# Optimization experiments

Hardware: AMD Instinct MI355X
Metric: run time of the kernel (lower is better)

## Reference

```python
import jax, jax.numpy as jnp
import numpy as np

N_NODES = 100000
N_EDGES = 3200000
IN_DIM = 256
HID_DIM = 64
OUT_DIM = 64


def setup_inputs() -> dict:
    key = jax.random.key(0)
    k1, k2, k3, k4, k5, k6 = jax.random.split(key, 6)
    x = jax.random.normal(k1, (N_NODES, IN_DIM), dtype=jnp.float32)
    edge_index = jax.random.randint(k2, (2, N_EDGES), 0, N_NODES, dtype=jnp.int32)
    # Glorot-style init for the two GCNConv layers (PyG default: glorot weight, zero bias)
    W1 = jax.random.normal(k3, (IN_DIM, HID_DIM), dtype=jnp.float32) * (1.0 / np.sqrt(IN_DIM))
    b1 = jnp.zeros((HID_DIM,), dtype=jnp.float32)
    W2 = jax.random.normal(k4, (HID_DIM, OUT_DIM), dtype=jnp.float32) * (1.0 / np.sqrt(HID_DIM))
    b2 = jnp.zeros((OUT_DIM,), dtype=jnp.float32)
    return {"x": x, "edge_index": edge_index, "W1": W1, "b1": b1, "W2": W2, "b2": b2}


def _gcn_conv(x, src, dst, deg_inv_sqrt, W, b, n):
    # PyG GCNConv: h = x W; out_i = sum_j norm_ij * h_j + b, with symmetric norm
    h = x @ W                                   # (n, d_out) small GEMM
    norm = deg_inv_sqrt[src] * deg_inv_sqrt[dst]  # (E+n,)
    msg = norm[:, None] * h[src]                # gather (E+n, d_out)
    agg = jax.ops.segment_sum(msg, dst, num_segments=n)  # scatter-add
    return agg + b


def reference(x, edge_index, W1, b1, W2, b2):
    n = x.shape[0]
    loops = jnp.arange(n, dtype=edge_index.dtype)
    src = jnp.concatenate([edge_index[0], loops])
    dst = jnp.concatenate([edge_index[1], loops])
    # degree on destination (col) with added self-loops, weight 1.0
    deg = jax.ops.segment_sum(jnp.ones_like(dst, dtype=x.dtype), dst, num_segments=n)
    deg_inv_sqrt = jnp.where(deg > 0, jax.lax.rsqrt(deg), 0.0)
    h = jax.nn.relu(_gcn_conv(x, src, dst, deg_inv_sqrt, W1, b1, n))
    return _gcn_conv(h, src, dst, deg_inv_sqrt, W2, b2, n)
```

## Files before the change

### kernel.cpp

```cpp
#include <hip/hip_runtime.h>
#include <cstdint>
#include <cstddef>


#define BIN_SHIFT 7
#define BIN_NODES 128
#define MAX_BINS 1024
#define SUP_SHIFT 11
#define FINE_PER_SUP 16
#define NSUP_MAX 64
#define SCAP 56
#define SRC_BITS 17
#define SRC_MASK ((1 << SRC_BITS) - 1)

typedef unsigned short ushort_t;

typedef __attribute__((ext_vector_type(8))) short bf16x8;
typedef __attribute__((ext_vector_type(4))) float f32x4;

union FragB {
  uint4 u;
  bf16x8 b;
};

__device__ __forceinline__ float4 bfq2f4(uint2 p) {
  float4 r;
  r.x = __uint_as_float(p.x << 16);
  r.y = __uint_as_float(p.x & 0xFFFF0000u);
  r.z = __uint_as_float(p.y << 16);
  r.w = __uint_as_float(p.y & 0xFFFF0000u);
  return r;
}
__device__ __forceinline__ unsigned f2bf(float f) {
  unsigned u = __float_as_uint(f);
  return (u + 0x7FFFu + ((u >> 16) & 1u)) >> 16;
}
__device__ __forceinline__ uint2 f42bfq(float4 f) {
  uint2 r;
  r.x = f2bf(f.x) | (f2bf(f.y) << 16);
  r.y = f2bf(f.z) | (f2bf(f.w) << 16);
  return r;
}

__global__ void zero_int(int* __restrict__ p, int n) {
  int i = blockIdx.x * blockDim.x + threadIdx.x;
  if (i < n) p[i] = 0;
}

__global__ __launch_bounds__(256) void bin_count(const int* __restrict__ dst, int E, int nbins,
                                                 int* __restrict__ binCnt) {
  __shared__ int h[MAX_BINS];
  for (int i = threadIdx.x; i < nbins; i += 256) h[i] = 0;
  __syncthreads();
  int stride = gridDim.x * 256;
  for (int e = blockIdx.x * 256 + threadIdx.x; e < E; e += stride)
    atomicAdd(&h[dst[e] >> BIN_SHIFT], 1);
  __syncthreads();
  for (int i = threadIdx.x; i < nbins; i += 256)
    if (h[i]) atomicAdd(&binCnt[i], h[i]);
}

__global__ __launch_bounds__(256) void bin_scan(const int* __restrict__ binCnt, int nbins, int E,
                                                int* __restrict__ binStart,
                                                int* __restrict__ binCursor,
                                                int* __restrict__ supCursor) {
  __shared__ int s[256];
  int t = threadIdx.x;
  int c[4];
  int sum = 0;
#pragma unroll
  for (int i = 0; i < 4; i++) {
    int idx = t * 4 + i;
    c[i] = (idx < nbins) ? binCnt[idx] : 0;
    sum += c[i];
  }
  int v = sum;
  s[t] = v;
  __syncthreads();
  for (int d = 1; d < 256; d <<= 1) {
    int add = (t >= d) ? s[t - d] : 0;
    __syncthreads();
    s[t] += add;
    __syncthreads();
  }
  int run = s[t] - v;
#pragma unroll
  for (int i = 0; i < 4; i++) {
    int idx = t * 4 + i;
    if (idx < nbins) {
      binStart[idx] = run;
      binCursor[idx] = run;
      if ((idx & (FINE_PER_SUP - 1)) == 0) supCursor[idx >> 4] = run;
      run += c[i];
    }
  }
  if (t == 0) binStart[nbins] = E;
}

__global__ __launch_bounds__(256) void super_fill(const int* __restrict__ src,
                                                  const int* __restrict__ dst, int E, int nsup,
                                                  int* __restrict__ supCursor,
                                                  unsigned* __restrict__ supbuf) {
  __shared__ unsigned stage[NSUP_MAX * SCAP];
  __shared__ int lcnt[NSUP_MAX], lbase[NSUP_MAX], lscan[NSUP_MAX + 1];
  const int tid = threadIdx.x;
  const int t0 = blockIdx.x * 2048;
  const int t1 = min(E, t0 + 2048);

  int dv[8], sv[8];
#pragma unroll
  for (int i = 0; i < 8; i++) {
    int e = t0 + i * 256 + tid;
    if (e < t1) {
      dv[i] = dst[e];
      sv[i] = src[e];
    }
  }
  if (tid < nsup) lcnt[tid] = 0;
  __syncthreads();
#pragma unroll
  for (int i = 0; i < 8; i++) {
    int e = t0 + i * 256 + tid;
    if (e < t1) {
      int d = dv[i];
      int sb = d >> SUP_SHIFT;
      unsigned v = ((unsigned)(d & ((1 << SUP_SHIFT) - 1)) << SRC_BITS) | (unsigned)sv[i];
      int idx = atomicAdd(&lcnt[sb], 1);
      if (idx < SCAP)
        stage[sb * SCAP + idx] = v;
      else {
        int g = atomicAdd(&supCursor[sb], 1);
        supbuf[g] = v;
      }
    }
  }
  __syncthreads();
  if (tid < nsup) {
    int c = min(lcnt[tid], SCAP);
    lcnt[tid] = c;
    lbase[tid] = c ? atomicAdd(&supCursor[tid], c) : 0;
  }
  __syncthreads();
  if (tid < 64) {
    int vv = (tid < nsup) ? lcnt[tid] : 0;
    int ss = vv;
#pragma unroll
    for (int d = 1; d < 64; d <<= 1) {
      int u = __shfl_up(ss, d);
      if (tid >= d) ss += u;
    }
    lscan[tid + 1] = ss;
    if (tid == 0) lscan[0] = 0;
  }
  __syncthreads();
  int total = lscan[nsup];
  for (int j = tid; j < total; j += 256) {
    int lo = 0, hi = nsup;
    while (hi - lo > 1) {
      int mid = (lo + hi) >> 1;
      if (lscan[mid] <= j)
        lo = mid;
      else
        hi = mid;
    }
    int off = j - lscan[lo];
    supbuf[lbase[lo] + off] = stage[lo * SCAP + off];
  }
}

__global__ __launch_bounds__(256) void fine_fill(const unsigned* __restrict__ supbuf,
                                                 const int* __restrict__ binStart, int nbins,
                                                 int* __restrict__ binCursor,
                                                 unsigned* __restrict__ binbuf) {
  __shared__ int lcnt[FINE_PER_SUP], lbase[FINE_PER_SUP];
  int sb = blockIdx.x >> 3, p = blockIdx.x & 7;
  int seg0 = binStart[sb << 4];
  int seg1 = binStart[min((sb + 1) << 4, nbins)];
  int part = (seg1 - seg0 + 7) >> 3;
  int c0 = seg0 + p * part;
  int c1 = min(seg1, c0 + part);
  if (threadIdx.x < FINE_PER_SUP) lcnt[threadIdx.x] = 0;
  __syncthreads();
  for (int i = c0 + threadIdx.x; i < c1; i += 256) atomicAdd(&lcnt[supbuf[i] >> 24], 1);
  __syncthreads();
  if (threadIdx.x < FINE_PER_SUP) {
    int c = lcnt[threadIdx.x];
    lbase[threadIdx.x] = c ? atomicAdd(&binCursor[(sb << 4) + threadIdx.x], c) : 0;
    lcnt[threadIdx.x] = 0;
  }
  __syncthreads();
  for (int i = c0 + threadIdx.x; i < c1; i += 256) {
    unsigned v = supbuf[i];
    unsigned dls = v >> SRC_BITS;
    int f = dls >> BIN_SHIFT;
    unsigned vf = ((dls & (BIN_NODES - 1)) << SRC_BITS) | (v & SRC_MASK);
    int idx = lbase[f] + atomicAdd(&lcnt[f], 1);
    binbuf[idx] = vf;
  }
}

__global__ __launch_bounds__(256) void node_count_dis(const unsigned* __restrict__ binbuf,
                                                      const int* __restrict__ binStart, int N,
                                                      int* __restrict__ count,
                                                      float* __restrict__ dis) {
  __shared__ int cnt[BIN_NODES];
  int b = blockIdx.x;
  int nodeBase = b << BIN_SHIFT;
  if (threadIdx.x < BIN_NODES) cnt[threadIdx.x] = 0;
  __syncthreads();
  int s0 = binStart[b], s1 = binStart[b + 1];
  for (int i = s0 + threadIdx.x; i < s1; i += 256) atomicAdd(&cnt[binbuf[i] >> SRC_BITS], 1);
  __syncthreads();
  if (threadIdx.x < BIN_NODES) {
    int node = nodeBase + threadIdx.x;
    if (node < N) {
      int c = cnt[threadIdx.x];
      count[node] = c;
      dis[node] = rsqrtf((float)(c + 1));
    }
  }
}

__global__ __launch_bounds__(256) void bin_csr(const unsigned* __restrict__ binbuf,
                                               const int* __restrict__ binStart,
                                               const int* __restrict__ count, int N, int E,
                                               int* __restrict__ rowptr, int* __restrict__ col) {
  __shared__ int cur[BIN_NODES];
  __shared__ int pref[BIN_NODES];
  int b = blockIdx.x, t = threadIdx.x;
  int nodeBase = b << BIN_SHIFT;
  int c = 0;
  if (t < BIN_NODES) {
    int node = nodeBase + t;
    c = (node < N) ? count[node] : 0;
    pref[t] = c;
  }
  __syncthreads();
  for (int d = 1; d < BIN_NODES; d <<= 1) {
    int add = (t < BIN_NODES && t >= d) ? pref[t - d] : 0;
    __syncthreads();
    if (t < BIN_NODES) pref[t] += add;
    __syncthreads();
  }
  int s0 = binStart[b];
  if (t < BIN_NODES) {
    int node = nodeBase + t;
    if (node < N) {
      int ex = s0 + pref[t] - c;
      rowptr[node] = ex;
      cur[t] = ex;
    }
  }
  if (b == 0 && t == 255) rowptr[N] = E;
  __syncthreads();
  int s1 = binStart[b + 1];
  for (int i = s0 + t; i < s1; i += 256) {
    unsigned v = binbuf[i];
    int slot = atomicAdd(&cur[v >> SRC_BITS], 1);
    col[slot] = v & SRC_MASK;
  }
}

__global__ __launch_bounds__(256) void wsplit(const float* __restrict__ W1,
                                              const float* __restrict__ W2,
                                              ushort_t* __restrict__ wt1,
                                              ushort_t* __restrict__ wt2) {
  int i = blockIdx.x * 256 + threadIdx.x;
  const float* W;
  ushort_t* wt;
  int K, idx;
  if (i < 256 * 64) {
    W = W1; wt = wt1; K = 256; idx = i;
  } else if (i < 256 * 64 + 64 * 64) {
    W = W2; wt = wt2; K = 64; idx = i - 256 * 64;
  } else
    return;
  int n = idx & 63, k = idx >> 6;
  float f = W[k * 64 + n];
  unsigned u = __float_as_uint(f);
  unsigned hb = u & 0xFFFF0000u;
  float lo = f - __uint_as_float(hb);
  wt[(size_t)n * K + k] = (ushort_t)(u >> 16);
  wt[(size_t)64 * K + (size_t)n * K + k] = (ushort_t)(__float_as_uint(lo) >> 16);
}

__device__ __forceinline__ void split8u(uint4 a, uint4 b, uint4& xh, uint4& xl) {
  unsigned ua[8] = {a.x, a.y, a.z, a.w, b.x, b.y, b.z, b.w};
  unsigned hw[4], lw[4];
#pragma unroll
  for (int p = 0; p < 4; p++) {
    unsigned u0 = ua[2 * p], u1 = ua[2 * p + 1];
    unsigned h0 = u0 & 0xFFFF0000u, h1 = u1 & 0xFFFF0000u;
    float l0 = __uint_as_float(u0) - __uint_as_float(h0);
    float l1 = __uint_as_float(u1) - __uint_as_float(h1);
    hw[p] = (u0 >> 16) | h1;
    lw[p] = (__float_as_uint(l0) >> 16) | (__float_as_uint(l1) & 0xFFFF0000u);
  }
  xh = make_uint4(hw[0], hw[1], hw[2], hw[3]);
  xl = make_uint4(lw[0], lw[1], lw[2], lw[3]);
}

__global__ __launch_bounds__(256, 3) void gemm1_mfma(const float* __restrict__ A,
                                                     const ushort_t* __restrict__ Wt,
                                                     uint2* __restrict__ Cb, int M) {
  constexpr int K = 256;
  __shared__ uint4 xtile[3][4][256];
  const int lane = threadIdx.x & 63;
  const int wv = threadIdx.x >> 6;
  const int l15 = lane & 15;
  const int lq = lane >> 4;
  const int m0 = blockIdx.x * 128 + wv * 32;

  const ushort_t* __restrict__ Wlo = Wt + (size_t)64 * K;

  f32x4 acc[2][4];
#pragma unroll
  for (int a = 0; a < 2; a++)
#pragma unroll
    for (int b = 0; b < 4; b++) acc[a][b] = (f32x4){0.f, 0.f, 0.f, 0.f};

  auto stage_tile = [&](int kt, int buf) {
#pragma unroll
    for (int c = 0; c < 4; c++) {
      int s = c * 64 + lane;
      int r = s >> 3;
      int c4 = (s & 7) ^ (r & 7);
      int nd = m0 + r;
      if (nd >= M) nd = M - 1;
      const float* gp = A + (size_t)nd * K + kt * 32 + c4 * 4;
      __builtin_amdgcn_global_load_lds(
          (const __attribute__((address_space(1))) void*)gp,
          (__attribute__((address_space(3))) void*)&xtile[buf][wv][c * 64], 16, 0, 0);
    }
  };

  stage_tile(0, 0);
  stage_tile(1, 1);
  __builtin_amdgcn_sched_barrier(0);

#pragma unroll
  for (int j = 0; j < 8; j++) {
    FragB w[8];
    {
      const int kb = j * 32 + lq * 8;
#pragma unroll
      for (int nt = 0; nt < 4; nt++) {
        w[nt].u = *(const uint4*)(Wt + (size_t)(nt * 16 + l15) * K + kb);
        w[4 + nt].u = *(const uint4*)(Wlo + (size_t)(nt * 16 + l15) * K + kb);
      }
    }
    __builtin_amdgcn_sched_barrier(0);
    if (j < 7)
      asm volatile("s_waitcnt vmcnt(12)" ::: "memory");
    else
      asm volatile("s_waitcnt vmcnt(8)" ::: "memory");
    __builtin_amdgcn_sched_barrier(0);
    uint4 xa[2][2];
#pragma unroll
    for (int mt = 0; mt < 2; mt++) {
      int mr = mt * 16 + l15;
#pragma unroll
      for (int hh = 0; hh < 2; hh++) {
        int c4 = (lq * 2 + hh) ^ (mr & 7);
        xa[mt][hh] = *(const uint4*)&xtile[j % 3][wv][mr * 8 + c4];
      }
    }
    __builtin_amdgcn_sched_barrier(0);
    if (j + 2 < 8) stage_tile(j + 2, (j + 2) % 3);
    __builtin_amdgcn_sched_barrier(0);
    FragB xh0, xl0, xh1, xl1;
    split8u(xa[0][0], xa[0][1], xh0.u, xl0.u);
    split8u(xa[1][0], xa[1][1], xh1.u, xl1.u);
#pragma unroll
    for (int nt = 0; nt < 4; nt++) {
      acc[0][nt] = __builtin_amdgcn_mfma_f32_16x16x32_bf16(w[nt].b, xh0.b, acc[0][nt], 0, 0, 0);
      acc[0][nt] = __builtin_amdgcn_mfma_f32_16x16x32_bf16(w[nt].b, xl0.b, acc[0][nt], 0, 0, 0);
      acc[1][nt] = __builtin_amdgcn_mfma_f32_16x16x32_bf16(w[nt].b, xh1.b, acc[1][nt], 0, 0, 0);
      acc[1][nt] = __builtin_amdgcn_mfma_f32_16x16x32_bf16(w[nt].b, xl1.b, acc[1][nt], 0, 0, 0);
    }
#pragma unroll
    for (int nt = 0; nt < 4; nt++) {
      acc[0][nt] = __builtin_amdgcn_mfma_f32_16x16x32_bf16(w[4 + nt].b, xh0.b, acc[0][nt], 0, 0, 0);
      acc[1][nt] = __builtin_amdgcn_mfma_f32_16x16x32_bf16(w[4 + nt].b, xh1.b, acc[1][nt], 0, 0, 0);
    }
  }

#pragma unroll
  for (int mt = 0; mt < 2; mt++) {
    int node = m0 + mt * 16 + l15;
    if (node < M) {
      uint2* cp = Cb + (size_t)node * 16 + lq;
#pragma unroll
      for (int nt = 0; nt < 4; nt++) {
        float4 o = make_float4(acc[mt][nt][0], acc[mt][nt][1], acc[mt][nt][2], acc[mt][nt][3]);
        cp[nt * 4] = f42bfq(o);
      }
    }
  }
}

__global__ __launch_bounds__(256, 3) void gemm2_mfma(const ushort_t* __restrict__ Av,
                                                     const ushort_t* __restrict__ Wt,
                                                     uint2* __restrict__ Cb, int M) {
  constexpr int K = 64;
  constexpr int NT = K / 32;
  const int lane = threadIdx.x & 63;
  const int wv = threadIdx.x >> 6;
  const int l15 = lane & 15;
  const int lq = lane >> 4;
  const int m0 = blockIdx.x * 128 + wv * 32;

  const ushort_t* __restrict__ Wlo = Wt + (size_t)64 * K;

  f32x4 acc[2][4];
#pragma unroll
  for (int a = 0; a < 2; a++)
#pragma unroll
    for (int b = 0; b < 4; b++) acc[a][b] = (f32x4){0.f, 0.f, 0.f, 0.f};

  int node[2], ncl[2];
#pragma unroll
  for (int mt = 0; mt < 2; mt++) {
    node[mt] = m0 + mt * 16 + l15;
    ncl[mt] = node[mt] < M ? node[mt] : (M - 1);
  }

  FragB xa[NT][2], wh[NT][4], wl[NT][4];
#pragma unroll
  for (int t = 0; t < NT; t++)
#pragma unroll
    for (int mt = 0; mt < 2; mt++)
      xa[t][mt].u = *(const uint4*)(Av + (size_t)ncl[mt] * K + t * 32 + lq * 8);
#pragma unroll
  for (int t = 0; t < NT; t++)
#pragma unroll
    for (int nt = 0; nt < 4; nt++) {
      wh[t][nt].u = *(const uint4*)(Wt + (size_t)(nt * 16 + l15) * K + t * 32 + lq * 8);
      wl[t][nt].u = *(const uint4*)(Wlo + (size_t)(nt * 16 + l15) * K + t * 32 + lq * 8);
    }
#pragma unroll
  for (int t = 0; t < NT; t++)
#pragma unroll
    for (int mt = 0; mt < 2; mt++)
#pragma unroll
      for (int nt = 0; nt < 4; nt++) {
        acc[mt][nt] =
            __builtin_amdgcn_mfma_f32_16x16x32_bf16(wh[t][nt].b, xa[t][mt].b, acc[mt][nt], 0, 0, 0);
        acc[mt][nt] =
            __builtin_amdgcn_mfma_f32_16x16x32_bf16(wl[t][nt].b, xa[t][mt].b, acc[mt][nt], 0, 0, 0);
      }

#pragma unroll
  for (int mt = 0; mt < 2; mt++) {
    if (node[mt] < M) {
      uint2* cp = Cb + (size_t)node[mt] * 16 + lq;
#pragma unroll
      for (int nt = 0; nt < 4; nt++) {
        float4 o = make_float4(acc[mt][nt][0], acc[mt][nt][1], acc[mt][nt][2], acc[mt][nt][3]);
        cp[nt * 4] = f42bfq(o);
      }
    }
  }
}

template <bool OUTBF>
__global__ __launch_bounds__(256) void agg_kernel(
    const uint2* __restrict__ h, const int* __restrict__ rowptr, const int* __restrict__ col,
    const float* __restrict__ dis, const float* __restrict__ bias, void* __restrict__ outv,
    int N, int relu) {
  int wid = (blockIdx.x * blockDim.x + threadIdx.x) >> 6;
  if (wid >= N) return;
  int lane = threadIdx.x & 63;
  int sub = lane & 15;
  int quarter = lane >> 4;

  int start = rowptr[wid], end = rowptr[wid + 1];
  float di = dis[wid];

  float4 a0 = make_float4(0.f, 0.f, 0.f, 0.f), a1 = a0, a2 = a0, a3 = a0;
  {
    float4 self = bfq2f4(h[(size_t)wid * 16 + sub]);
    if (quarter == 0) {
      a0.x = di * self.x;
      a0.y = di * self.y;
      a0.z = di * self.z;
      a0.w = di * self.w;
    }
  }

  for (int base = start; base < end; base += 64) {
    int e = base + lane;
    int sj = 0;
    float wj = 0.f;
    if (e < end) {
      sj = col[e];
      wj = dis[sj];
    }
    int cnt = end - base;
    if (cnt > 64) cnt = 64;
    int rounds = (cnt + 3) >> 2;

    uint2 g0, g1, g2, g3;
    float w0, w1, w2, w3;
#define ISSUE(gi, G, W)                                              \
  do {                                                               \
    int _i = (4 * (gi) + quarter) & 63;                              \
    int _s = __shfl(sj, _i);                                         \
    float _w = __shfl(wj, _i);                                       \
    if ((gi) < rounds) {                                             \
      G = h[(size_t)_s * 16 + sub];                                  \
      W = _w;                                                        \
    } else {                                                         \
      G = make_uint2(0u, 0u);                                        \
      W = 0.f;                                                       \
    }                                                                \
  } while (0)

    ISSUE(0, g0, w0);
    ISSUE(1, g1, w1);
    ISSUE(2, g2, w2);
    ISSUE(3, g3, w3);
    int rounds4 = (rounds + 3) & ~3;
    for (int t0 = 0; t0 < rounds4; t0 += 4) {
      {
        float4 gf = bfq2f4(g0);
        a0.x += w0 * gf.x; a0.y += w0 * gf.y; a0.z += w0 * gf.z; a0.w += w0 * gf.w;
      }
      ISSUE(t0 + 4, g0, w0);
      {
        float4 gf = bfq2f4(g1);
        a1.x += w1 * gf.x; a1.y += w1 * gf.y; a1.z += w1 * gf.z; a1.w += w1 * gf.w;
      }
      ISSUE(t0 + 5, g1, w1);
      {
        float4 gf = bfq2f4(g2);
        a2.x += w2 * gf.x; a2.y += w2 * gf.y; a2.z += w2 * gf.z; a2.w += w2 * gf.w;
      }
      ISSUE(t0 + 6, g2, w2);
      {
        float4 gf = bfq2f4(g3);
        a3.x += w3 * gf.x; a3.y += w3 * gf.y; a3.z += w3 * gf.z; a3.w += w3 * gf.w;
      }
      ISSUE(t0 + 7, g3, w3);
    }
#undef ISSUE
  }

  float sx = (a0.x + a1.x) + (a2.x + a3.x);
  float sy = (a0.y + a1.y) + (a2.y + a3.y);
  float sz = (a0.z + a1.z) + (a2.z + a3.z);
  float sw = (a0.w + a1.w) + (a2.w + a3.w);
  sx += __shfl_down(sx, 32); sy += __shfl_down(sy, 32);
  sz += __shfl_down(sz, 32); sw += __shfl_down(sw, 32);
  sx += __shfl_down(sx, 16); sy += __shfl_down(sy, 16);
  sz += __shfl_down(sz, 16); sw += __shfl_down(sw, 16);
  if (quarter == 0) {
    float4 bv = ((const float4*)bias)[sub];
    float4 o = make_float4(di * sx + bv.x, di * sy + bv.y, di * sz + bv.z, di * sw + bv.w);
    if (relu) {
      o.x = fmaxf(o.x, 0.f);
      o.y = fmaxf(o.y, 0.f);
      o.z = fmaxf(o.z, 0.f);
      o.w = fmaxf(o.w, 0.f);
    }
    if (OUTBF)
      ((uint2*)outv)[(size_t)wid * 16 + sub] = f42bfq(o);
    else
      ((float4*)outv)[(size_t)wid * 16 + sub] = o;
  }
}

extern "C" void kernel_launch(void* const* d_in, const int* in_sizes, int n_in,
                              void* d_out, int out_size, void* d_ws, size_t ws_size,
                              hipStream_t stream) {
  const float* x = (const float*)d_in[0];
  const int* ei = (const int*)d_in[1];
  const float* W1 = (const float*)d_in[2];
  const float* b1 = (const float*)d_in[3];
  const float* W2 = (const float*)d_in[4];
  const float* b2 = (const float*)d_in[5];

  const int IN = 256;
  const int E = in_sizes[1] / 2;
  const int N = in_sizes[0] / IN;
  const int* src = ei;
  const int* dst = ei + E;
  const int nbins = (N + BIN_NODES - 1) >> BIN_SHIFT;
  const int nsup = (N + (1 << SUP_SHIFT) - 1) >> SUP_SHIFT;

  char* ws = (char*)d_ws;
  size_t off = 0;
  auto alloc = [&](size_t bytes) -> void* {
    void* p = ws + off;
    off += (bytes + 255) & ~(size_t)255;
    return p;
  };
  int* count = (int*)alloc((size_t)N * 4);
  int* rowptr = (int*)alloc((size_t)(N + 1) * 4);
  float* dis = (float*)alloc((size_t)N * 4);
  int* binCnt = (int*)alloc(MAX_BINS * 4);
  int* binStart = (int*)alloc((MAX_BINS + 1) * 4);
  int* binCursor = (int*)alloc(MAX_BINS * 4);
  int* supCursor = (int*)alloc(NSUP_MAX * 4);
  int* col = (int*)alloc((size_t)E * 4);
  unsigned* supbuf = (unsigned*)col;
  uint2* out1 = (uint2*)alloc((size_t)N * 64 * 2);
  size_t big = ((size_t)E * 4 > (size_t)N * 128) ? (size_t)E * 4 : (size_t)N * 128;
  unsigned* binbuf = (unsigned*)alloc(big);
  uint2* h = (uint2*)binbuf;
  ushort_t* wt1 = (ushort_t*)alloc((size_t)2 * 64 * 256 * 2);
  ushort_t* wt2 = (ushort_t*)alloc((size_t)2 * 64 * 64 * 2);
  float* outf = (float*)d_out;

  zero_int<<<(nbins + 255) / 256, 256, 0, stream>>>(binCnt, nbins);
  bin_count<<<1024, 256, 0, stream>>>(dst, E, nbins, binCnt);
  bin_scan<<<1, 256, 0, stream>>>(binCnt, nbins, E, binStart, binCursor, supCursor);
  super_fill<<<(E + 2047) / 2048, 256, 0, stream>>>(src, dst, E, nsup, supCursor, supbuf);
  fine_fill<<<nsup * 8, 256, 0, stream>>>(supbuf, binStart, nbins, binCursor, binbuf);
  node_count_dis<<<nbins, 256, 0, stream>>>(binbuf, binStart, N, count, dis);
  bin_csr<<<nbins, 256, 0, stream>>>(binbuf, binStart, count, N, E, rowptr, col);
  wsplit<<<(256 * 64 + 64 * 64 + 255) / 256, 256, 0, stream>>>(W1, W2, wt1, wt2);

  gemm1_mfma<<<(N + 127) / 128, 256, 0, stream>>>(x, wt1, h, N);
  agg_kernel<true><<<(N + 3) / 4, 256, 0, stream>>>(h, rowptr, col, dis, b1, out1, N, 1);
  gemm2_mfma<<<(N + 127) / 128, 256, 0, stream>>>((const ushort_t*)out1, wt2, h, N);
  agg_kernel<false><<<(N + 3) / 4, 256, 0, stream>>>(h, rowptr, col, dis, b2, outf, N, 0);
}
```

Before: 461.3 us.

## Fuse node count into CSR build and shrink GEMM row tiles to 16 per wave

Merges node_count_dis into bin_csr, so per-node counts are computed in shared memory and the count array plus one kernel launch and one pass over binbuf are removed. Both MFMA GEMM kernels now give each wave 16 rows instead of 32 and each block 64 rows, with half-size LDS tiles and launch bounds raised to 4 blocks per CU. The smaller tiles are meant to add occupancy and blocks for latency hiding, at the cost of reloading the weight fragments for twice as many blocks and less reuse of each weight load.

```diff
diff --git a/kernel.cpp b/kernel.cpp
--- a/kernel.cpp
+++ b/kernel.cpp
@@ -199,40 +199,27 @@
   }
 }
 
-__global__ __launch_bounds__(256) void node_count_dis(const unsigned* __restrict__ binbuf,
-                                                      const int* __restrict__ binStart, int N,
-                                                      int* __restrict__ count,
-                                                      float* __restrict__ dis) {
+__global__ __launch_bounds__(256) void bin_csr(const unsigned* __restrict__ binbuf,
+                                               const int* __restrict__ binStart, int N, int E,
+                                               int* __restrict__ rowptr, int* __restrict__ col,
+                                               float* __restrict__ dis) {
   __shared__ int cnt[BIN_NODES];
-  int b = blockIdx.x;
-  int nodeBase = b << BIN_SHIFT;
-  if (threadIdx.x < BIN_NODES) cnt[threadIdx.x] = 0;
-  __syncthreads();
-  int s0 = binStart[b], s1 = binStart[b + 1];
-  for (int i = s0 + threadIdx.x; i < s1; i += 256) atomicAdd(&cnt[binbuf[i] >> SRC_BITS], 1);
-  __syncthreads();
-  if (threadIdx.x < BIN_NODES) {
-    int node = nodeBase + threadIdx.x;
-    if (node < N) {
-      int c = cnt[threadIdx.x];
-      count[node] = c;
-      dis[node] = rsqrtf((float)(c + 1));
-    }
-  }
-}
-
-__global__ __launch_bounds__(256) void bin_csr(const unsigned* __restrict__ binbuf,
-                                               const int* __restrict__ binStart,
-                                               const int* __restrict__ count, int N, int E,
-                                               int* __restrict__ rowptr, int* __restrict__ col) {
   __shared__ int cur[BIN_NODES];
   __shared__ int pref[BIN_NODES];
   int b = blockIdx.x, t = threadIdx.x;
   int nodeBase = b << BIN_SHIFT;
+  if (t < BIN_NODES) cnt[t] = 0;
+  __syncthreads();
+  int s0 = binStart[b], s1 = binStart[b + 1];
+  for (int i = s0 + t; i < s1; i += 256) atomicAdd(&cnt[binbuf[i] >> SRC_BITS], 1);
+  __syncthreads();
   int c = 0;
   if (t < BIN_NODES) {
     int node = nodeBase + t;
-    c = (node < N) ? count[node] : 0;
+    if (node < N) {
+      c = cnt[t];
+      dis[node] = rsqrtf((float)(c + 1));
+    }
     pref[t] = c;
   }
   __syncthreads();
@@ -242,7 +229,6 @@
     if (t < BIN_NODES) pref[t] += add;
     __syncthreads();
   }
-  int s0 = binStart[b];
   if (t < BIN_NODES) {
     int node = nodeBase + t;
     if (node < N) {
@@ -253,7 +239,6 @@
   }
   if (b == 0 && t == 255) rowptr[N] = E;
   __syncthreads();
-  int s1 = binStart[b + 1];
   for (int i = s0 + t; i < s1; i += 256) {
     unsigned v = binbuf[i];
     int slot = atomicAdd(&cur[v >> SRC_BITS], 1);
@@ -300,28 +285,26 @@
   xl = make_uint4(lw[0], lw[1], lw[2], lw[3]);
 }
 
-__global__ __launch_bounds__(256, 3) void gemm1_mfma(const float* __restrict__ A,
+__global__ __launch_bounds__(256, 4) void gemm1_mfma(const float* __restrict__ A,
                                                      const ushort_t* __restrict__ Wt,
                                                      uint2* __restrict__ Cb, int M) {
   constexpr int K = 256;
-  __shared__ uint4 xtile[3][4][256];
+  __shared__ uint4 xtile[3][4][128];
   const int lane = threadIdx.x & 63;
   const int wv = threadIdx.x >> 6;
   const int l15 = lane & 15;
   const int lq = lane >> 4;
-  const int m0 = blockIdx.x * 128 + wv * 32;
+  const int m0 = blockIdx.x * 64 + wv * 16;
 
   const ushort_t* __restrict__ Wlo = Wt + (size_t)64 * K;
 
-  f32x4 acc[2][4];
-#pragma unroll
-  for (int a = 0; a < 2; a++)
-#pragma unroll
-    for (int b = 0; b < 4; b++) acc[a][b] = (f32x4){0.f, 0.f, 0.f, 0.f};
+  f32x4 acc[4];
+#pragma unroll
+  for (int b = 0; b < 4; b++) acc[b] = (f32x4){0.f, 0.f, 0.f, 0.f};
 
   auto stage_tile = [&](int kt, int buf) {
 #pragma unroll
-    for (int c = 0; c < 4; c++) {
+    for (int c = 0; c < 2; c++) {
       int s = c * 64 + lane;
       int r = s >> 3;
       int c4 = (s & 7) ^ (r & 7);
@@ -351,55 +334,46 @@
     }
     __builtin_amdgcn_sched_barrier(0);
     if (j < 7)
-      asm volatile("s_waitcnt vmcnt(12)" ::: "memory");
+      asm volatile("s_waitcnt vmcnt(10)" ::: "memory");
     else
       asm volatile("s_waitcnt vmcnt(8)" ::: "memory");
     __builtin_amdgcn_sched_barrier(0);
-    uint4 xa[2][2];
-#pragma unroll
-    for (int mt = 0; mt < 2; mt++) {
-      int mr = mt * 16 + l15;
-#pragma unroll
-      for (int hh = 0; hh < 2; hh++) {
-        int c4 = (lq * 2 + hh) ^ (mr & 7);
-        xa[mt][hh] = *(const uint4*)&xtile[j % 3][wv][mr * 8 + c4];
-      }
+    uint4 xa[2];
+#pragma unroll
+    for (int hh = 0; hh < 2; hh++) {
+      int c4 = (lq * 2 + hh) ^ (l15 & 7);
+      xa[hh] = *(const uint4*)&xtile[j % 3][wv][l15 * 8 + c4];
     }
     __builtin_amdgcn_sched_barrier(0);
     if (j + 2 < 8) stage_tile(j + 2, (j + 2) % 3);
     __builtin_amdgcn_sched_barrier(0);
-    FragB xh0, xl0, xh1, xl1;
-    split8u(xa[0][0], xa[0][1], xh0.u, xl0.u);
-    split8u(xa[1][0], xa[1][1], xh1.u, xl1.u);
+    FragB xh0, xl0;
+    split8u(xa[0], xa[1], xh0.u, xl0.u);
 #pragma unroll
     for (int nt = 0; nt < 4; nt++) {
-      acc[0][nt] = __builtin_amdgcn_mfma_f32_16x16x32_bf16(w[nt].b, xh0.b, acc[0][nt], 0, 0, 0);
-      acc[0][nt] = __builtin_amdgcn_mfma_f32_16x16x32_bf16(w[nt].b, xl0.b, acc[0][nt], 0, 0, 0);
-      acc[1][nt] = __builtin_amdgcn_mfma_f32_16x16x32_bf16(w[nt].b, xh1.b, acc[1][nt], 0, 0, 0);
-      acc[1][nt] = __builtin_amdgcn_mfma_f32_16x16x32_bf16(w[nt].b, xl1.b, acc[1][nt], 0, 0, 0);
+      acc[nt] = __builtin_amdgcn_mfma_f32_16x16x32_bf16(w[nt].b, xh0.b, acc[nt], 0, 0, 0);
+      acc[nt] = __builtin_amdgcn_mfma_f32_16x16x32_bf16(w[nt].b, xl0.b, acc[nt], 0, 0, 0);
     }
 #pragma unroll
     for (int nt = 0; nt < 4; nt++) {
-      acc[0][nt] = __builtin_amdgcn_mfma_f32_16x16x32_bf16(w[4 + nt].b, xh0.b, acc[0][nt], 0, 0, 0);
-      acc[1][nt] = __builtin_amdgcn_mfma_f32_16x16x32_bf16(w[4 + nt].b, xh1.b, acc[1][nt], 0, 0, 0);
-    }
-  }
-
-#pragma unroll
-  for (int mt = 0; mt < 2; mt++) {
-    int node = m0 + mt * 16 + l15;
+      acc[nt] = __builtin_amdgcn_mfma_f32_16x16x32_bf16(w[4 + nt].b, xh0.b, acc[nt], 0, 0, 0);
+    }
+  }
+
+  {
+    int node = m0 + l15;
     if (node < M) {
       uint2* cp = Cb + (size_t)node * 16 + lq;
 #pragma unroll
       for (int nt = 0; nt < 4; nt++) {
-        float4 o = make_float4(acc[mt][nt][0], acc[mt][nt][1], acc[mt][nt][2], acc[mt][nt][3]);
+        float4 o = make_float4(acc[nt][0], acc[nt][1], acc[nt][2], acc[nt][3]);
         cp[nt * 4] = f42bfq(o);
       }
     }
   }
 }
 
-__global__ __launch_bounds__(256, 3) void gemm2_mfma(const ushort_t* __restrict__ Av,
+__global__ __launch_bounds__(256, 4) void gemm2_mfma(const ushort_t* __restrict__ Av,
                                                      const ushort_t* __restrict__ Wt,
                                                      uint2* __restrict__ Cb, int M) {
   constexpr int K = 64;
@@ -408,29 +382,21 @@
   const int wv = threadIdx.x >> 6;
   const int l15 = lane & 15;
   const int lq = lane >> 4;
-  const int m0 = blockIdx.x * 128 + wv * 32;
+  const int m0 = blockIdx.x * 64 + wv * 16;
 
   const ushort_t* __restrict__ Wlo = Wt + (size_t)64 * K;
 
-  f32x4 acc[2][4];
-#pragma unroll
-  for (int a = 0; a < 2; a++)
-#pragma unroll
-    for (int b = 0; b < 4; b++) acc[a][b] = (f32x4){0.f, 0.f, 0.f, 0.f};
-
-  int node[2], ncl[2];
-#pragma unroll
-  for (int mt = 0; mt < 2; mt++) {
-    node[mt] = m0 + mt * 16 + l15;
-    ncl[mt] = node[mt] < M ? node[mt] : (M - 1);
-  }
-
-  FragB xa[NT][2], wh[NT][4], wl[NT][4];
+  f32x4 acc[4];
+#pragma unroll
+  for (int b = 0; b < 4; b++) acc[b] = (f32x4){0.f, 0.f, 0.f, 0.f};
+
+  int node = m0 + l15;
+  int ncl = node < M ? node : (M - 1);
+
+  FragB xa[NT], wh[NT][4], wl[NT][4];
 #pragma unroll
   for (int t = 0; t < NT; t++)
-#pragma unroll
-    for (int mt = 0; mt < 2; mt++)
-      xa[t][mt].u = *(const uint4*)(Av + (size_t)ncl[mt] * K + t * 32 + lq * 8);
+    xa[t].u = *(const uint4*)(Av + (size_t)ncl * K + t * 32 + lq * 8);
 #pragma unroll
   for (int t = 0; t < NT; t++)
 #pragma unroll
@@ -441,24 +407,17 @@
 #pragma unroll
   for (int t = 0; t < NT; t++)
 #pragma unroll
-    for (int mt = 0; mt < 2; mt++)
-#pragma unroll
-      for (int nt = 0; nt < 4; nt++) {
-        acc[mt][nt] =
-            __builtin_amdgcn_mfma_f32_16x16x32_bf16(wh[t][nt].b, xa[t][mt].b, acc[mt][nt], 0, 0, 0);
-        acc[mt][nt] =
-            __builtin_amdgcn_mfma_f32_16x16x32_bf16(wl[t][nt].b, xa[t][mt].b, acc[mt][nt], 0, 0, 0);
-      }
-
-#pragma unroll
-  for (int mt = 0; mt < 2; mt++) {
-    if (node[mt] < M) {
-      uint2* cp = Cb + (size_t)node[mt] * 16 + lq;
-#pragma unroll
-      for (int nt = 0; nt < 4; nt++) {
-        float4 o = make_float4(acc[mt][nt][0], acc[mt][nt][1], acc[mt][nt][2], acc[mt][nt][3]);
-        cp[nt * 4] = f42bfq(o);
-      }
+    for (int nt = 0; nt < 4; nt++) {
+      acc[nt] = __builtin_amdgcn_mfma_f32_16x16x32_bf16(wh[t][nt].b, xa[t].b, acc[nt], 0, 0, 0);
+      acc[nt] = __builtin_amdgcn_mfma_f32_16x16x32_bf16(wl[t][nt].b, xa[t].b, acc[nt], 0, 0, 0);
+    }
+
+  if (node < M) {
+    uint2* cp = Cb + (size_t)node * 16 + lq;
+#pragma unroll
+    for (int nt = 0; nt < 4; nt++) {
+      float4 o = make_float4(acc[nt][0], acc[nt][1], acc[nt][2], acc[nt][3]);
+      cp[nt * 4] = f42bfq(o);
     }
   }
 }
@@ -595,7 +554,6 @@
     off += (bytes + 255) & ~(size_t)255;
     return p;
   };
-  int* count = (int*)alloc((size_t)N * 4);
   int* rowptr = (int*)alloc((size_t)(N + 1) * 4);
   float* dis = (float*)alloc((size_t)N * 4);
   int* binCnt = (int*)alloc(MAX_BINS * 4);
@@ -617,12 +575,11 @@
   bin_scan<<<1, 256, 0, stream>>>(binCnt, nbins, E, binStart, binCursor, supCursor);
   super_fill<<<(E + 2047) / 2048, 256, 0, stream>>>(src, dst, E, nsup, supCursor, supbuf);
   fine_fill<<<nsup * 8, 256, 0, stream>>>(supbuf, binStart, nbins, binCursor, binbuf);
-  node_count_dis<<<nbins, 256, 0, stream>>>(binbuf, binStart, N, count, dis);
-  bin_csr<<<nbins, 256, 0, stream>>>(binbuf, binStart, count, N, E, rowptr, col);
+  bin_csr<<<nbins, 256, 0, stream>>>(binbuf, binStart, N, E, rowptr, col, dis);
   wsplit<<<(256 * 64 + 64 * 64 + 255) / 256, 256, 0, stream>>>(W1, W2, wt1, wt2);
 
-  gemm1_mfma<<<(N + 127) / 128, 256, 0, stream>>>(x, wt1, h, N);
+  gemm1_mfma<<<(N + 63) / 64, 256, 0, stream>>>(x, wt1, h, N);
   agg_kernel<true><<<(N + 3) / 4, 256, 0, stream>>>(h, rowptr, col, dis, b1, out1, N, 1);
-  gemm2_mfma<<<(N + 127) / 128, 256, 0, stream>>>((const ushort_t*)out1, wt2, h, N);
+  gemm2_mfma<<<(N + 63) / 64, 256, 0, stream>>>((const ushort_t*)out1, wt2, h, N);
   agg_kernel<false><<<(N + 3) / 4, 256, 0, stream>>>(h, rowptr, col, dis, b2, outf, N, 0);
 }
```

Result: slower. 477.2 us (+3.5%).

## Fuse degree count into CSR build and enlarge gemm1 tile to 256 rows

Applied to the files above, without the earlier changes.

Merges the node_count_dis kernel into bin_csr, so per-node counts are computed in shared memory and the count array round trip and one launch go away. gemm1 now processes 64 rows per wave (256 per block), reusing each weight fragment across four M-tiles instead of two. It switches from triple to double buffering with an explicit LDS wait before restaging, and lowers the occupancy hint to two blocks. This costs more registers and less latency hiding per block, in exchange for fewer weight reloads per row.

```diff
diff --git a/kernel.cpp b/kernel.cpp
--- a/kernel.cpp
+++ b/kernel.cpp
@@ -199,40 +199,27 @@
   }
 }
 
-__global__ __launch_bounds__(256) void node_count_dis(const unsigned* __restrict__ binbuf,
-                                                      const int* __restrict__ binStart, int N,
-                                                      int* __restrict__ count,
-                                                      float* __restrict__ dis) {
+__global__ __launch_bounds__(256) void bin_csr(const unsigned* __restrict__ binbuf,
+                                               const int* __restrict__ binStart, int N, int E,
+                                               int* __restrict__ rowptr, int* __restrict__ col,
+                                               float* __restrict__ dis) {
   __shared__ int cnt[BIN_NODES];
-  int b = blockIdx.x;
-  int nodeBase = b << BIN_SHIFT;
-  if (threadIdx.x < BIN_NODES) cnt[threadIdx.x] = 0;
-  __syncthreads();
-  int s0 = binStart[b], s1 = binStart[b + 1];
-  for (int i = s0 + threadIdx.x; i < s1; i += 256) atomicAdd(&cnt[binbuf[i] >> SRC_BITS], 1);
-  __syncthreads();
-  if (threadIdx.x < BIN_NODES) {
-    int node = nodeBase + threadIdx.x;
-    if (node < N) {
-      int c = cnt[threadIdx.x];
-      count[node] = c;
-      dis[node] = rsqrtf((float)(c + 1));
-    }
-  }
-}
-
-__global__ __launch_bounds__(256) void bin_csr(const unsigned* __restrict__ binbuf,
-                                               const int* __restrict__ binStart,
-                                               const int* __restrict__ count, int N, int E,
-                                               int* __restrict__ rowptr, int* __restrict__ col) {
   __shared__ int cur[BIN_NODES];
   __shared__ int pref[BIN_NODES];
   int b = blockIdx.x, t = threadIdx.x;
   int nodeBase = b << BIN_SHIFT;
+  if (t < BIN_NODES) cnt[t] = 0;
+  __syncthreads();
+  int s0 = binStart[b], s1 = binStart[b + 1];
+  for (int i = s0 + t; i < s1; i += 256) atomicAdd(&cnt[binbuf[i] >> SRC_BITS], 1);
+  __syncthreads();
   int c = 0;
   if (t < BIN_NODES) {
     int node = nodeBase + t;
-    c = (node < N) ? count[node] : 0;
+    if (node < N) {
+      c = cnt[t];
+      dis[node] = rsqrtf((float)(c + 1));
+    }
     pref[t] = c;
   }
   __syncthreads();
@@ -242,7 +229,6 @@
     if (t < BIN_NODES) pref[t] += add;
     __syncthreads();
   }
-  int s0 = binStart[b];
   if (t < BIN_NODES) {
     int node = nodeBase + t;
     if (node < N) {
@@ -253,7 +239,6 @@
   }
   if (b == 0 && t == 255) rowptr[N] = E;
   __syncthreads();
-  int s1 = binStart[b + 1];
   for (int i = s0 + t; i < s1; i += 256) {
     unsigned v = binbuf[i];
     int slot = atomicAdd(&cur[v >> SRC_BITS], 1);
@@ -300,28 +285,28 @@
   xl = make_uint4(lw[0], lw[1], lw[2], lw[3]);
 }
 
-__global__ __launch_bounds__(256, 3) void gemm1_mfma(const float* __restrict__ A,
+__global__ __launch_bounds__(256, 2) void gemm1_mfma(const float* __restrict__ A,
                                                      const ushort_t* __restrict__ Wt,
                                                      uint2* __restrict__ Cb, int M) {
   constexpr int K = 256;
-  __shared__ uint4 xtile[3][4][256];
+  __shared__ uint4 xtile[2][4][512];
   const int lane = threadIdx.x & 63;
   const int wv = threadIdx.x >> 6;
   const int l15 = lane & 15;
   const int lq = lane >> 4;
-  const int m0 = blockIdx.x * 128 + wv * 32;
+  const int m0 = blockIdx.x * 256 + wv * 64;
 
   const ushort_t* __restrict__ Wlo = Wt + (size_t)64 * K;
 
-  f32x4 acc[2][4];
-#pragma unroll
-  for (int a = 0; a < 2; a++)
+  f32x4 acc[4][4];
+#pragma unroll
+  for (int a = 0; a < 4; a++)
 #pragma unroll
     for (int b = 0; b < 4; b++) acc[a][b] = (f32x4){0.f, 0.f, 0.f, 0.f};
 
   auto stage_tile = [&](int kt, int buf) {
 #pragma unroll
-    for (int c = 0; c < 4; c++) {
+    for (int c = 0; c < 8; c++) {
       int s = c * 64 + lane;
       int r = s >> 3;
       int c4 = (s & 7) ^ (r & 7);
@@ -351,42 +336,44 @@
     }
     __builtin_amdgcn_sched_barrier(0);
     if (j < 7)
-      asm volatile("s_waitcnt vmcnt(12)" ::: "memory");
+      asm volatile("s_waitcnt vmcnt(16)" ::: "memory");
     else
       asm volatile("s_waitcnt vmcnt(8)" ::: "memory");
     __builtin_amdgcn_sched_barrier(0);
-    uint4 xa[2][2];
-#pragma unroll
-    for (int mt = 0; mt < 2; mt++) {
+    uint4 xa[4][2];
+#pragma unroll
+    for (int mt = 0; mt < 4; mt++) {
       int mr = mt * 16 + l15;
 #pragma unroll
       for (int hh = 0; hh < 2; hh++) {
         int c4 = (lq * 2 + hh) ^ (mr & 7);
-        xa[mt][hh] = *(const uint4*)&xtile[j % 3][wv][mr * 8 + c4];
+        xa[mt][hh] = *(const uint4*)&xtile[j & 1][wv][mr * 8 + c4];
       }
     }
     __builtin_amdgcn_sched_barrier(0);
-    if (j + 2 < 8) stage_tile(j + 2, (j + 2) % 3);
+    asm volatile("s_waitcnt lgkmcnt(0)" ::: "memory");
     __builtin_amdgcn_sched_barrier(0);
-    FragB xh0, xl0, xh1, xl1;
-    split8u(xa[0][0], xa[0][1], xh0.u, xl0.u);
-    split8u(xa[1][0], xa[1][1], xh1.u, xl1.u);
-#pragma unroll
-    for (int nt = 0; nt < 4; nt++) {
-      acc[0][nt] = __builtin_amdgcn_mfma_f32_16x16x32_bf16(w[nt].b, xh0.b, acc[0][nt], 0, 0, 0);
-      acc[0][nt] = __builtin_amdgcn_mfma_f32_16x16x32_bf16(w[nt].b, xl0.b, acc[0][nt], 0, 0, 0);
-      acc[1][nt] = __builtin_amdgcn_mfma_f32_16x16x32_bf16(w[nt].b, xh1.b, acc[1][nt], 0, 0, 0);
-      acc[1][nt] = __builtin_amdgcn_mfma_f32_16x16x32_bf16(w[nt].b, xl1.b, acc[1][nt], 0, 0, 0);
-    }
-#pragma unroll
-    for (int nt = 0; nt < 4; nt++) {
-      acc[0][nt] = __builtin_amdgcn_mfma_f32_16x16x32_bf16(w[4 + nt].b, xh0.b, acc[0][nt], 0, 0, 0);
-      acc[1][nt] = __builtin_amdgcn_mfma_f32_16x16x32_bf16(w[4 + nt].b, xh1.b, acc[1][nt], 0, 0, 0);
-    }
-  }
-
-#pragma unroll
-  for (int mt = 0; mt < 2; mt++) {
+    if (j + 2 < 8) stage_tile(j + 2, j & 1);
+    __builtin_amdgcn_sched_barrier(0);
+#pragma unroll
+    for (int mt = 0; mt < 4; mt++) {
+      FragB xh, xl;
+      split8u(xa[mt][0], xa[mt][1], xh.u, xl.u);
+#pragma unroll
+      for (int nt = 0; nt < 4; nt++) {
+        acc[mt][nt] = __builtin_amdgcn_mfma_f32_16x16x32_bf16(w[nt].b, xh.b, acc[mt][nt], 0, 0, 0);
+        acc[mt][nt] = __builtin_amdgcn_mfma_f32_16x16x32_bf16(w[nt].b, xl.b, acc[mt][nt], 0, 0, 0);
+      }
+#pragma unroll
+      for (int nt = 0; nt < 4; nt++) {
+        acc[mt][nt] =
+            __builtin_amdgcn_mfma_f32_16x16x32_bf16(w[4 + nt].b, xh.b, acc[mt][nt], 0, 0, 0);
+      }
+    }
+  }
+
+#pragma unroll
+  for (int mt = 0; mt < 4; mt++) {
     int node = m0 + mt * 16 + l15;
     if (node < M) {
       uint2* cp = Cb + (size_t)node * 16 + lq;
@@ -595,7 +582,6 @@
     off += (bytes + 255) & ~(size_t)255;
     return p;
   };
-  int* count = (int*)alloc((size_t)N * 4);
   int* rowptr = (int*)alloc((size_t)(N + 1) * 4);
   float* dis = (float*)alloc((size_t)N * 4);
   int* binCnt = (int*)alloc(MAX_BINS * 4);
@@ -617,11 +603,10 @@
   bin_scan<<<1, 256, 0, stream>>>(binCnt, nbins, E, binStart, binCursor, supCursor);
   super_fill<<<(E + 2047) / 2048, 256, 0, stream>>>(src, dst, E, nsup, supCursor, supbuf);
   fine_fill<<<nsup * 8, 256, 0, stream>>>(supbuf, binStart, nbins, binCursor, binbuf);
-  node_count_dis<<<nbins, 256, 0, stream>>>(binbuf, binStart, N, count, dis);
-  bin_csr<<<nbins, 256, 0, stream>>>(binbuf, binStart, count, N, E, rowptr, col);
+  bin_csr<<<nbins, 256, 0, stream>>>(binbuf, binStart, N, E, rowptr, col, dis);
   wsplit<<<(256 * 64 + 64 * 64 + 255) / 256, 256, 0, stream>>>(W1, W2, wt1, wt2);
 
-  gemm1_mfma<<<(N + 127) / 128, 256, 0, stream>>>(x, wt1, h, N);
+  gemm1_mfma<<<(N + 255) / 256, 256, 0, stream>>>(x, wt1, h, N);
   agg_kernel<true><<<(N + 3) / 4, 256, 0, stream>>>(h, rowptr, col, dis, b1, out1, N, 1);
   gemm2_mfma<<<(N + 127) / 128, 256, 0, stream>>>((const ushort_t*)out1, wt2, h, N);
   agg_kernel<false><<<(N + 3) / 4, 256, 0, stream>>>(h, rowptr, col, dis, b2, outf, N, 0);
```

Result: no change. 453.6 us (-1.7%).
